# Kernel tuning notes

Hardware: AMD Instinct MI355X
Metric: run time of the kernel (lower is better)

Reference implementation:

```python
import jax, jax.numpy as jnp
import numpy as np

BEV_H = 200
BEV_W = 200
H_METERS = 100.0
W_METERS = 100.0
THRESHOLD = 0.05
LOW_PASS = 0.3  # 3DGS screen-space low-pass filter added to cov2D diagonal
ALPHA_MIN = 1.0 / 255.0
ALPHA_MAX = 0.99


def setup_inputs() -> dict:
    key = jax.random.key(0)
    k1, k2, k3, k4 = jax.random.split(key, 4)
    B, G, D = 2, 2000, 32
    features = jax.random.normal(k1, (B, G, D), dtype=jnp.float32)
    # means uniformly covering the [-50, 50] x [-50, 50] BEV extent (z unused)
    means3D = (jax.random.uniform(k2, (B, G, 3), dtype=jnp.float32) - 0.5) * 100.0
    # PSD 3x3 covariances, ~1-2 m std -> a few pixels at 2 px/m
    A = jax.random.normal(k3, (B, G, 3, 3), dtype=jnp.float32)
    Sigma = jnp.einsum('bgij,bgkj->bgik', A, A) + 0.1 * jnp.eye(3, dtype=jnp.float32)
    iu = jnp.triu_indices(3)
    cov3D = Sigma[:, :, iu[0], iu[1]]  # b g 6 : (xx, xy, xz, yy, yz, zz)
    opacities = jax.random.uniform(k4, (B, G, 1), dtype=jnp.float32)
    return {'features': features, 'means3D': means3D, 'cov3D': cov3D,
            'opacities': opacities}


def _render(features, means3D, cov3D, opacities):
    B, G, D = features.shape
    sh = BEV_H / H_METERS  # 2 px / m
    sw = BEV_W / W_METERS
    op = opacities[..., 0]                      # b g
    mask = op > THRESHOLD                       # opacity gating (torch masks rows;
                                                # zero-alpha is mathematically identical)
    # orthographic BEV projection (full_proj_transform rows 0 and 1)
    x, y = means3D[..., 0], means3D[..., 1]
    u = -sh * y + BEV_H / 2.0                   # row coordinate, b g
    v = -sw * x + BEV_W / 2.0                   # col coordinate, b g
    # cov2D = M Sigma M^T with M = [[0, sh, 0], [sw, 0, 0]], plus low-pass
    sxx, sxy, syy = cov3D[..., 0], cov3D[..., 1], cov3D[..., 3]
    c00 = sh * sh * syy + LOW_PASS
    c01 = sh * sw * sxy
    c11 = sw * sw * sxx + LOW_PASS
    det = c00 * c11 - c01 * c01
    valid = mask & (det > 0.0)
    inv_det = jnp.where(det > 0.0, 1.0 / jnp.where(det > 0.0, det, 1.0), 0.0)
    cA = c11 * inv_det                          # conic (A, B, C)
    cB = -c01 * inv_det
    cC = c00 * inv_det
    # per-pixel Gaussian power, separably broadcast: [b g H 1] + [b g 1 W]
    gi = jnp.arange(BEV_H, dtype=jnp.float32)
    gj = jnp.arange(BEV_W, dtype=jnp.float32)
    du = u[..., None] - gi                      # b g H
    dv = v[..., None] - gj                      # b g W
    power = (-0.5 * cA)[..., None, None] * (du * du)[..., :, None] \
          + (-0.5 * cC)[..., None, None] * (dv * dv)[..., None, :] \
          + (-cB)[..., None, None] * du[..., :, None] * dv[..., None, :]  # b g H W
    alpha = jnp.minimum(ALPHA_MAX, op[..., None, None] * jnp.exp(power))
    keep = valid[..., None, None] & (power <= 0.0) & (alpha >= ALPHA_MIN)
    alpha = jnp.where(keep, alpha, 0.0)
    alpha = alpha.reshape(B, G, BEV_H * BEV_W)  # b g p
    # front-to-back alpha compositing: exclusive cumprod of transmittance
    T_excl = jnp.concatenate(
        [jnp.ones((B, 1, BEV_H * BEV_W), dtype=alpha.dtype),
         jnp.cumprod(1.0 - alpha, axis=1)[:, :-1]], axis=1)
    weight = alpha * T_excl                     # b g p
    out = jnp.einsum('bgp,bgd->bdp', weight, features)  # bg_color is zeros
    out = out.reshape(B, D, BEV_H, BEV_W)
    num_gaussians = jnp.mean(jnp.sum(mask.astype(jnp.float32), axis=1))
    return out, num_gaussians


def reference(features, means3D, cov3D, opacities):
    return _render(features, means3D, cov3D, opacities)
```

## Files before the change

kernel.cpp:

```cpp
#include <hip/hip_runtime.h>
#include <math.h>

#define BEV_H 200
#define BEV_W 200
#define NPIX (BEV_H * BEV_W)
#define TILE 8
#define NT 25
#define NB 2
#define T_DEAD 1e-10f
#define SEGCAP 512
#define KC 32
#define NLOG255 (-5.5412635f)

__device__ __forceinline__ unsigned pk2bf(float x, float y)
{
    unsigned ux = __float_as_uint(x), uy = __float_as_uint(y);
    ux = ux + 0x7fffu + ((ux >> 16) & 1u);
    uy = uy + 0x7fffu + ((uy >> 16) & 1u);
    return (ux >> 16) | (uy & 0xffff0000u);
}

__global__ __launch_bounds__(256) void render_fused_kernel(
    const float* __restrict__ features, const float* __restrict__ means3D,
    const float* __restrict__ cov3D, const float* __restrict__ opac,
    float* __restrict__ out, int G)
{
    __shared__ int    glist[4][SEGCAP];
    __shared__ float4 plA[4][KC];
    __shared__ float2 plB[4][KC];
    __shared__ uint4  flq[4][KC][4];
    __shared__ float  xch[2][64][33];

    const int tid  = threadIdx.x;
    const int lane = tid & 63;
    const int w    = tid >> 6;
    const int b  = blockIdx.z;
    const int tj = blockIdx.x;
    const int ti = blockIdx.y;
    const int j = tj * TILE + (lane & 7);
    const int i = ti * TILE + (lane >> 3);
    const float fi = (float)i, fj = (float)j;
    const float ti_lo = (float)(ti * TILE), ti_hi = ti_lo + (TILE - 1);
    const float tj_lo = (float)(tj * TILE), tj_hi = tj_lo + (TILE - 1);
    const int gbase = b * G;
    const int g_lo = (w * G) >> 2;
    const int g_hi = ((w + 1) * G) >> 2;
    const int rounds = (g_hi - g_lo + 63) >> 6;

    int tot = 0;
    {
        int gg = min(g_lo + lane, g_hi - 1);
        size_t gi = (size_t)(gbase + gg);
        float x0 = means3D[gi * 3 + 0], y0 = means3D[gi * 3 + 1];
        float s0 = cov3D[gi * 6 + 0], s1 = cov3D[gi * 6 + 1], s3 = cov3D[gi * 6 + 3];
        float o0 = opac[gi];
        for (int r = 0; r < rounds; ++r) {
            float x1 = 0.f, y1 = 0.f, t0 = 0.f, t1 = 0.f, t3 = 0.f, o1 = 0.f;
            if (r + 1 < rounds) {
                const int gn = min(g_lo + (r + 1) * 64 + lane, g_hi - 1);
                const size_t gni = (size_t)(gbase + gn);
                x1 = means3D[gni * 3 + 0]; y1 = means3D[gni * 3 + 1];
                t0 = cov3D[gni * 6 + 0];   t1 = cov3D[gni * 6 + 1];
                t3 = cov3D[gni * 6 + 3];   o1 = opac[gni];
            }
            const int g = g_lo + r * 64 + lane;
            const float u = -2.0f * y0 + 100.0f;
            const float v = -2.0f * x0 + 100.0f;
            const float c00 = 4.0f * s3 + 0.3f;
            const float c01 = 4.0f * s1;
            const float c11 = 4.0f * s0 + 0.3f;
            const float det = c00 * c11 - c01 * c01;
            bool keep = false;
            if (o0 > 0.05f && det > 0.0f && g < g_hi) {
                const float L = __logf(255.0f * o0);
                const float ru = sqrtf(2.0f * L * c00) + 0.01f;
                const float rv = sqrtf(2.0f * L * c11) + 0.01f;
                keep = (u + ru >= ti_lo) && (u - ru <= ti_hi) &&
                       (v + rv >= tj_lo) && (v - rv <= tj_hi);
            }
            const unsigned long long bal = __ballot(keep);
            if (keep) {
                const int pre = (int)__popcll(bal & ((1ull << lane) - 1ull));
                glist[w][tot + pre] = g;
            }
            tot += (int)__popcll(bal);
            x0 = x1; y0 = y1; s0 = t0; s1 = t1; s3 = t3; o0 = o1;
        }
    }

    float acc[32];
#pragma unroll
    for (int d = 0; d < 32; ++d) acc[d] = 0.0f;
    float T = 1.0f;

    for (int k0 = 0; k0 < tot; k0 += KC) {
        if (!__any(T >= T_DEAD)) break;
        const int nk = min(KC, tot - k0);

        if (lane < nk) {
            const int g = glist[w][k0 + lane];
            const size_t gi = (size_t)(gbase + g);
            const float x = means3D[gi * 3 + 0], y = means3D[gi * 3 + 1];
            const float sxx = cov3D[gi * 6 + 0], sxy = cov3D[gi * 6 + 1],
                        syy = cov3D[gi * 6 + 3];
            const float op = opac[gi];
            const float u = -2.0f * y + 100.0f;
            const float v = -2.0f * x + 100.0f;
            const float c00 = 4.0f * syy + 0.3f;
            const float c01 = 4.0f * sxy;
            const float c11 = 4.0f * sxx + 0.3f;
            const float inv = 1.0f / (c00 * c11 - c01 * c01);
            plA[w][lane] = make_float4(u, v, -0.5f * c11 * inv, c01 * inv);
            plB[w][lane] = make_float2(-0.5f * c00 * inv, __logf(op));
        }
        for (int idx = lane; idx < nk * 4; idx += 64) {
            const int e = idx >> 2, q = idx & 3;
            const int g = glist[w][k0 + e];
            const float4* fp =
                (const float4*)(features + (size_t)(gbase + g) * 32) + q * 2;
            const float4 A = fp[0], Bq = fp[1];
            flq[w][e][q] = make_uint4(pk2bf(A.x, A.y), pk2bf(A.z, A.w),
                                      pk2bf(Bq.x, Bq.y), pk2bf(Bq.z, Bq.w));
        }

#pragma unroll 2
        for (int k = 0; k < nk; ++k) {
            const float4 pA = plA[w][k];
            const float2 pB = plB[w][k];
            const float du = pA.x - fi;
            const float dv = pA.y - fj;
            const float power = pA.z * du * du + pB.x * dv * dv + pA.w * du * dv;
            const float powb = power + pB.y;
            float alpha = fminf(0.99f, __expf(powb));
            const bool ok = (powb >= NLOG255) && (power <= 0.0f);
            alpha = ok ? alpha : 0.0f;
            const float wgt = alpha * T;
            T *= 1.0f - alpha;
#pragma unroll
            for (int q = 0; q < 4; ++q) {
                const uint4 uq = flq[w][k][q];
                const unsigned uu[4] = {uq.x, uq.y, uq.z, uq.w};
#pragma unroll
                for (int c = 0; c < 4; ++c) {
                    const float lo = __uint_as_float(uu[c] << 16);
                    const float hi = __uint_as_float(uu[c] & 0xffff0000u);
                    acc[q * 8 + c * 2 + 0] = fmaf(wgt, lo, acc[q * 8 + c * 2 + 0]);
                    acc[q * 8 + c * 2 + 1] = fmaf(wgt, hi, acc[q * 8 + c * 2 + 1]);
                }
            }
        }
    }

    if (w == 1 || w == 3) {
        float* row = xch[(w - 1) >> 1][lane];
#pragma unroll
        for (int d = 0; d < 32; ++d) row[d] = acc[d];
        row[32] = T;
    }
    __syncthreads();
    if (w == 0 || w == 2) {
        const float* row = xch[w >> 1][lane];
        const float Tn = row[32];
#pragma unroll
        for (int d = 0; d < 32; ++d) acc[d] = fmaf(T, row[d], acc[d]);
        T *= Tn;
    }
    __syncthreads();
    if (w == 2) {
        float* row = xch[0][lane];
#pragma unroll
        for (int d = 0; d < 32; ++d) row[d] = acc[d];
        row[32] = T;
    }
    __syncthreads();

    if (w == 0) {
        const float* row = xch[0][lane];
#pragma unroll
        for (int d = 0; d < 32; ++d) acc[d] = fmaf(T, row[d], acc[d]);

        const int p = i * BEV_W + j;
        float* ob = out + (size_t)b * 32 * NPIX + p;
#pragma unroll
        for (int d = 0; d < 32; ++d) ob[(size_t)d * NPIX] = acc[d];
    }

    if (w == 1 && blockIdx.x == 0 && blockIdx.y == 0 && blockIdx.z == 0) {
        const float4* o4 = (const float4*)opac;
        const int n4 = (NB * G) >> 2;
        float s = 0.0f;
        for (int idx = lane; idx < n4; idx += 64) {
            const float4 o = o4[idx];
            s += (o.x > 0.05f ? 1.0f : 0.0f) + (o.y > 0.05f ? 1.0f : 0.0f) +
                 (o.z > 0.05f ? 1.0f : 0.0f) + (o.w > 0.05f ? 1.0f : 0.0f);
        }
#pragma unroll
        for (int off = 32; off > 0; off >>= 1) s += __shfl_down(s, off);
        if (lane == 0) out[NB * 32 * NPIX] = s * (1.0f / NB);
    }
}

extern "C" void kernel_launch(void* const* d_in, const int* in_sizes, int n_in,
                              void* d_out, int out_size, void* d_ws, size_t ws_size,
                              hipStream_t stream)
{
    const float* features = (const float*)d_in[0];
    const float* means3D  = (const float*)d_in[1];
    const float* cov3D    = (const float*)d_in[2];
    const float* opac     = (const float*)d_in[3];
    float* out = (float*)d_out;

    const int G = in_sizes[3] / NB;

    dim3 grid(NT, NT, NB);
    render_fused_kernel<<<grid, 256, 0, stream>>>(features, means3D, cov3D, opac,
                                                  out, G);
}
```

Baseline: 84.01 us.

## Precompute conic params during culling and shrink shared memory for occupancy

During the culling pass, the conic parameters for the first PCAP kept Gaussians per wave are now written straight to shared memory, so the main loop skips the global reload and recompute for those chunks. The gaussian list is stored as 16-bit indices and all shared arrays are packed into one aliased 24 KB buffer, with the exchange area overlaying the list. The launch bounds now request 5 blocks per CU, aiming at higher occupancy. The aliasing requires an extra barrier before the reduction, and the occupancy hint may force register spills given the 32-float accumulator.

```diff
diff --git a/kernel.cpp b/kernel.cpp
--- a/kernel.cpp
+++ b/kernel.cpp
@@ -9,6 +9,7 @@
 #define NB 2
 #define T_DEAD 1e-10f
 #define SEGCAP 512
+#define PCAP 128
 #define KC 32
 #define NLOG255 (-5.5412635f)
 
@@ -20,16 +21,17 @@
     return (ux >> 16) | (uy & 0xffff0000u);
 }
 
-__global__ __launch_bounds__(256) void render_fused_kernel(
+__global__ __launch_bounds__(256, 5) void render_fused_kernel(
     const float* __restrict__ features, const float* __restrict__ means3D,
     const float* __restrict__ cov3D, const float* __restrict__ opac,
     float* __restrict__ out, int G)
 {
-    __shared__ int    glist[4][SEGCAP];
-    __shared__ float4 plA[4][KC];
-    __shared__ float2 plB[4][KC];
-    __shared__ uint4  flq[4][KC][4];
-    __shared__ float  xch[2][64][33];
+    __shared__ __align__(16) unsigned char smem[24576];
+    unsigned short* glist = (unsigned short*)smem;
+    float4* plA = (float4*)(smem + 4096);
+    float2* plB = (float2*)(smem + 12288);
+    uint4*  flq = (uint4*)(smem + 16384);
+    float*  xch = (float*)smem;
 
     const int tid  = threadIdx.x;
     const int lane = tid & 63;
@@ -71,8 +73,9 @@
             const float c11 = 4.0f * s0 + 0.3f;
             const float det = c00 * c11 - c01 * c01;
             bool keep = false;
+            float L = 0.0f;
             if (o0 > 0.05f && det > 0.0f && g < g_hi) {
-                const float L = __logf(255.0f * o0);
+                L = __logf(255.0f * o0);
                 const float ru = sqrtf(2.0f * L * c00) + 0.01f;
                 const float rv = sqrtf(2.0f * L * c11) + 0.01f;
                 keep = (u + ru >= ti_lo) && (u - ru <= ti_hi) &&
@@ -80,8 +83,15 @@
             }
             const unsigned long long bal = __ballot(keep);
             if (keep) {
-                const int pre = (int)__popcll(bal & ((1ull << lane) - 1ull));
-                glist[w][tot + pre] = g;
+                const int slot = tot + (int)__popcll(bal & ((1ull << lane) - 1ull));
+                glist[w * SEGCAP + slot] = (unsigned short)g;
+                if (slot < PCAP) {
+                    const float inv = 1.0f / det;
+                    plA[w * PCAP + slot] =
+                        make_float4(u, v, -0.5f * c11 * inv, c01 * inv);
+                    plB[w * PCAP + slot] = make_float2(-0.5f * c00 * inv,
+                                                       L + NLOG255);
+                }
             }
             tot += (int)__popcll(bal);
             x0 = x1; y0 = y1; s0 = t0; s1 = t1; s3 = t3; o0 = o1;
@@ -97,8 +107,8 @@
         if (!__any(T >= T_DEAD)) break;
         const int nk = min(KC, tot - k0);
 
-        if (lane < nk) {
-            const int g = glist[w][k0 + lane];
+        if (k0 >= PCAP && lane < nk) {
+            const int g = glist[w * SEGCAP + k0 + lane];
             const size_t gi = (size_t)(gbase + g);
             const float x = means3D[gi * 3 + 0], y = means3D[gi * 3 + 1];
             const float sxx = cov3D[gi * 6 + 0], sxy = cov3D[gi * 6 + 1],
@@ -110,23 +120,23 @@
             const float c01 = 4.0f * sxy;
             const float c11 = 4.0f * sxx + 0.3f;
             const float inv = 1.0f / (c00 * c11 - c01 * c01);
-            plA[w][lane] = make_float4(u, v, -0.5f * c11 * inv, c01 * inv);
-            plB[w][lane] = make_float2(-0.5f * c00 * inv, __logf(op));
+            plA[w * PCAP + lane] = make_float4(u, v, -0.5f * c11 * inv, c01 * inv);
+            plB[w * PCAP + lane] = make_float2(-0.5f * c00 * inv, __logf(op));
         }
         for (int idx = lane; idx < nk * 4; idx += 64) {
             const int e = idx >> 2, q = idx & 3;
-            const int g = glist[w][k0 + e];
+            const int g = glist[w * SEGCAP + k0 + e];
             const float4* fp =
                 (const float4*)(features + (size_t)(gbase + g) * 32) + q * 2;
             const float4 A = fp[0], Bq = fp[1];
-            flq[w][e][q] = make_uint4(pk2bf(A.x, A.y), pk2bf(A.z, A.w),
-                                      pk2bf(Bq.x, Bq.y), pk2bf(Bq.z, Bq.w));
-        }
-
-#pragma unroll 2
+            flq[(w * KC + e) * 4 + q] = make_uint4(pk2bf(A.x, A.y), pk2bf(A.z, A.w),
+                                                   pk2bf(Bq.x, Bq.y), pk2bf(Bq.z, Bq.w));
+        }
+
+        const int pbase = w * PCAP + ((k0 < PCAP) ? k0 : 0);
         for (int k = 0; k < nk; ++k) {
-            const float4 pA = plA[w][k];
-            const float2 pB = plB[w][k];
+            const float4 pA = plA[pbase + k];
+            const float2 pB = plB[pbase + k];
             const float du = pA.x - fi;
             const float dv = pA.y - fj;
             const float power = pA.z * du * du + pB.x * dv * dv + pA.w * du * dv;
@@ -138,7 +148,7 @@
             T *= 1.0f - alpha;
 #pragma unroll
             for (int q = 0; q < 4; ++q) {
-                const uint4 uq = flq[w][k][q];
+                const uint4 uq = flq[(w * KC + k) * 4 + q];
                 const unsigned uu[4] = {uq.x, uq.y, uq.z, uq.w};
 #pragma unroll
                 for (int c = 0; c < 4; ++c) {
@@ -151,15 +161,16 @@
         }
     }
 
+    __syncthreads();
     if (w == 1 || w == 3) {
-        float* row = xch[(w - 1) >> 1][lane];
+        float* row = xch + (((w - 1) >> 1) * 64 + lane) * 33;
 #pragma unroll
         for (int d = 0; d < 32; ++d) row[d] = acc[d];
         row[32] = T;
     }
     __syncthreads();
     if (w == 0 || w == 2) {
-        const float* row = xch[w >> 1][lane];
+        const float* row = xch + ((w >> 1) * 64 + lane) * 33;
         const float Tn = row[32];
 #pragma unroll
         for (int d = 0; d < 32; ++d) acc[d] = fmaf(T, row[d], acc[d]);
@@ -167,7 +178,7 @@
     }
     __syncthreads();
     if (w == 2) {
-        float* row = xch[0][lane];
+        float* row = xch + lane * 33;
 #pragma unroll
         for (int d = 0; d < 32; ++d) row[d] = acc[d];
         row[32] = T;
@@ -175,7 +186,7 @@
     __syncthreads();
 
     if (w == 0) {
-        const float* row = xch[0][lane];
+        const float* row = xch + lane * 33;
 #pragma unroll
         for (int d = 0; d < 32; ++d) acc[d] = fmaf(T, row[d], acc[d]);
 
```

After: 82.44 us. No clear change (-1.9%).
